# Performance work log

Measured on AMD Instinct MI355X. Metric: run time of the kernel, lower is better.

Reference implementation:

```python
import jax, jax.numpy as jnp
import numpy as np

N_NODES = 20000
N_EDGES = 320000
IN_F = 16
OUT_F = 16
EDGE_DIM = 16
EDGE_HID = 64
BN_EPS = 1e-5


def setup_inputs() -> dict:
    key = jax.random.key(0)
    ks = jax.random.split(key, 12)
    inp = {
        "h_neigh": jax.random.normal(ks[0], (N_NODES, IN_F), dtype=jnp.float32),
        "h_self": jax.random.normal(ks[1], (N_NODES, IN_F), dtype=jnp.float32),
        "edge_features": jax.random.normal(ks[2], (N_EDGES, EDGE_DIM), dtype=jnp.float32),
        "src": jax.random.randint(ks[3], (N_EDGES,), 0, N_NODES),
        "dst": jax.random.randint(ks[4], (N_EDGES,), 0, N_NODES),
        # params (xavier-ish scale)
        "W_self": jax.random.normal(ks[5], (IN_F, OUT_F), dtype=jnp.float32) * (2.0 / (IN_F + OUT_F)) ** 0.5,
        "bn_gamma": jnp.ones((OUT_F,), dtype=jnp.float32),
        "bn_beta": jnp.zeros((OUT_F,), dtype=jnp.float32),
        "We1": jax.random.normal(ks[6], (EDGE_DIM, EDGE_HID), dtype=jnp.float32) * (2.0 / (EDGE_DIM + EDGE_HID)) ** 0.5,
        "be1": jnp.zeros((EDGE_HID,), dtype=jnp.float32),
        "We2": jax.random.normal(ks[7], (EDGE_HID, IN_F * OUT_F), dtype=jnp.float32) * (2.0 / (EDGE_HID + IN_F * OUT_F)) ** 0.5,
        "be2": jnp.zeros((IN_F * OUT_F,), dtype=jnp.float32),
    }
    return inp


def reference(h_neigh, h_self, edge_features, src, dst,
              W_self, bn_gamma, bn_beta, We1, be1, We2, be2):
    n_nodes = h_self.shape[0]
    in_f, out_f = W_self.shape
    # edge MLP -> per-edge weight matrix [E, in_f, out_f]
    eh = jax.nn.relu(edge_features @ We1 + be1)
    edge_w = (eh @ We2 + be2).reshape(-1, in_f, out_f)
    # gather src features, per-edge matvec, scatter-sum to dst
    # (sum over in_f commutes with the edge sum-reduce, matching
    #  update_all(u_mul_e, sum) followed by .sum(dim=1))
    msg = jnp.einsum('ei,eio->eo', h_neigh[src], edge_w)  # [E, out_f]
    neigh = jax.ops.segment_sum(msg, dst, num_segments=n_nodes)  # [N, out_f]
    # fc_self: Linear(no bias) -> BatchNorm1d (training stats) -> tanh
    y = h_self @ W_self
    mu = y.mean(axis=0)
    var = y.var(axis=0)
    y = (y - mu) / jnp.sqrt(var + BN_EPS) * bn_gamma + bn_beta
    y = jnp.tanh(y)
    z = jax.nn.relu(y + neigh)
    z_norm = jnp.linalg.norm(z, axis=1, keepdims=True)
    z_norm = jnp.where(z_norm == 0, jnp.ones_like(z_norm), z_norm)
    return z / z_norm
```

## Files before the change

kernel.cpp:

```cpp
#include <hip/hip_runtime.h>
#include <hip/hip_bf16.h>
#include <math.h>

#define NN 20000
#define NE 320000
#define BN_EPS 1e-5f
#define CAP 48
#define CNTP 16

#define MSG_BYTES   (NE * 16 * 4)
#define ELIST_OFF   MSG_BYTES
#define ELIST_BYTES (NN * CAP * 4)
#define CNT_OFF     (ELIST_OFF + ELIST_BYTES)
#define CNT_BYTES   (NN * CNTP * 4)
#define BNACC_OFF   (CNT_OFF + CNT_BYTES)
#define Y_OFF       (BNACC_OFF + 128)
#define ZERO_OFF    CNT_OFF
#define ZERO_BYTES  (CNT_BYTES + 128)

typedef _Float16 f16x8 __attribute__((ext_vector_type(8)));
typedef float    f32x4 __attribute__((ext_vector_type(4)));

union H8 { f16x8 v; unsigned short us[8]; unsigned int ui[4]; };

__device__ __forceinline__ unsigned short f2h(float f) {
    _Float16 h = (_Float16)f;
    return __builtin_bit_cast(unsigned short, h);
}
__device__ __forceinline__ unsigned int pack2h(float a, float b) {
    return (unsigned int)f2h(a) | ((unsigned int)f2h(b) << 16);
}

__global__ __launch_bounds__(256) void bucket_kernel(
    const int* __restrict__ dst, int* __restrict__ elist, int* __restrict__ cntp)
{
    int i = (int)blockIdx.x * 256 + (int)threadIdx.x;
    if (i < NE) {
        int d0 = dst[i];
        int k0 = atomicAdd(&cntp[d0 * CNTP], 1);
        if (k0 < CAP) elist[d0 * CAP + k0] = i;
    }
}

__global__ __launch_bounds__(256, 3) void edge_kernel(
    const float* __restrict__ h_neigh, const float* __restrict__ efeat,
    const int* __restrict__ src,
    const float* __restrict__ We1, const float* __restrict__ be1,
    const float* __restrict__ We2, const float* __restrict__ be2,
    float* __restrict__ msgb,
    const float* __restrict__ h_self, const float* __restrict__ Wsf,
    float* __restrict__ y, float* __restrict__ bnacc)
{
    __shared__ __align__(16) unsigned short A3sw[16 * 2 * 64 * 8];
    __shared__ float red[4][32];

    const int t = threadIdx.x;

    {
#pragma unroll
        for (int i = 0; i < 8; i++) {
            int R = t + 256 * i;
            int co = R & 15;
            int g  = (R >> 4) & 3;
            int mbkb = R >> 6;
            int mb = mbkb >> 1, kb = mbkb & 1;
            const float* wp = We2 + (size_t)(kb * 32 + g * 8) * 256 + mb * 16 + co;
            H8 h8;
#pragma unroll
            for (int j = 0; j < 8; j++)
                h8.us[j] = f2h(wp[j * 256]);
            *(f16x8*)&A3sw[R * 8] = h8.v;
        }
    }
    __syncthreads();

    const int L = t & 63, wv = t >> 6;
    const int lo16 = L & 15, q = L >> 4;
    const int qc = q & 1;
    const bool qlow = (q < 2);
    const bool qhi1 = ((q >> 1) != 0);

    H8 w1[4];
#pragma unroll
    for (int c = 0; c < 4; c++) {
#pragma unroll
        for (int j = 0; j < 8; j++) {
            float w;
            if (q < 2)                 w = We1[(q * 8 + j) * 64 + c * 16 + lo16];
            else if (q == 2 && j == 0) w = be1[c * 16 + lo16];
            else                       w = 0.f;
            w1[c].us[j] = f2h(w);
        }
    }

    H8 be2T;
#pragma unroll
    for (int j = 0; j < 8; j++) {
        float bv = be2[(qc * 8 + j) * 16 + lo16];
        be2T.us[j] = qlow ? f2h(bv) : (unsigned short)0;
    }

    const int addrA = (((q & 1) * 2 + 0) * 16 + lo16) * 4;
    const int addrB = (((q & 1) * 2 + 1) * 16 + lo16) * 4;

    const int NT = NE / 64;
    int bt = blockIdx.x;
    {
        int e = bt * 64 + wv * 16 + lo16;
        int se = src[e];
        const float4* ep0 = (const float4*)(efeat + (size_t)e * 16 + qc * 8);
        float4 efA = ep0[0], efB = ep0[1];
        float xr[16];
        {
            const float4* xp = (const float4*)(h_neigh + (size_t)se * 16);
#pragma unroll
            for (int k4 = 0; k4 < 4; k4++) {
                float4 a = xp[k4];
                xr[k4*4+0] = a.x; xr[k4*4+1] = a.y; xr[k4*4+2] = a.z; xr[k4*4+3] = a.w;
            }
        }

        while (true) {
            int btn = bt + gridDim.x;
            bool hn = btn < NT;
            int en = 0, sen = 0;
            float4 efAn = efA, efBn = efB;
            if (hn) {
                en = btn * 64 + wv * 16 + lo16;
                sen = src[en];
                const float4* epn = (const float4*)(efeat + (size_t)en * 16 + qc * 8);
                efAn = epn[0]; efBn = epn[1];
            }

            H8 a2;
            {
                float ev[8] = {efA.x, efA.y, efA.z, efA.w, efB.x, efB.y, efB.z, efB.w};
#pragma unroll
                for (int j = 0; j < 8; j++) {
                    if (qlow) {
                        a2.us[j] = f2h(ev[j]);
                    } else {
                        a2.us[j] = (q == 2 && j == 0) ? (unsigned short)0x3C00 : (unsigned short)0;
                    }
                }
            }

            float vch[4][4];
#pragma unroll
            for (int c = 0; c < 4; c++) {
                f32x4 c2 = {0.f, 0.f, 0.f, 0.f};
                c2 = __builtin_amdgcn_mfma_f32_16x16x32_f16(w1[c].v, a2.v, c2, 0, 0, 0);
#pragma unroll
                for (int r = 0; r < 4; r++) vch[c][r] = fmaxf(c2[r], 0.f);
            }

            unsigned int dw[4][2];
#pragma unroll
            for (int c = 0; c < 4; c++) {
#pragma unroll
                for (int d = 0; d < 2; d++)
                    dw[c][d] = pack2h(vch[c][2*d], vch[c][2*d+1]);
            }

            H8 b3[2];
#pragma unroll
            for (int kb = 0; kb < 2; kb++) {
#pragma unroll
                for (int tt = 0; tt < 4; tt++) {
                    int d = tt & 1;
                    int addr = (tt >> 1) ? addrB : addrA;
                    int h0 = __builtin_amdgcn_ds_bpermute(addr, (int)dw[kb*2+0][d]);
                    int h1 = __builtin_amdgcn_ds_bpermute(addr, (int)dw[kb*2+1][d]);
                    b3[kb].ui[tt] = (unsigned int)(qhi1 ? h1 : h0);
                }
            }

            float4 nx0 = make_float4(0.f, 0.f, 0.f, 0.f), nx1 = nx0, nx2 = nx0, nx3 = nx0;
            if (hn) {
                const float4* xpn = (const float4*)(h_neigh + (size_t)sen * 16);
                nx0 = xpn[0]; nx1 = xpn[1]; nx2 = xpn[2]; nx3 = xpn[3];
            }

            H8 xT;
#pragma unroll
            for (int j = 0; j < 8; j++)
                xT.us[j] = qlow ? f2h(xr[qc * 8 + j]) : (unsigned short)0;
            f32x4 msg = {0.f, 0.f, 0.f, 0.f};
            msg = __builtin_amdgcn_mfma_f32_16x16x32_f16(be2T.v, xT.v, msg, 0, 0, 0);

#pragma unroll 4
            for (int mb = 0; mb < 16; mb++) {
                f16x8 a3a = *(const f16x8*)&A3sw[((mb * 2 + 0) * 64 + L) * 8];
                f16x8 a3b = *(const f16x8*)&A3sw[((mb * 2 + 1) * 64 + L) * 8];
                f32x4 acc = {0.f, 0.f, 0.f, 0.f};
                acc = __builtin_amdgcn_mfma_f32_16x16x32_f16(a3a, b3[0].v, acc, 0, 0, 0);
                acc = __builtin_amdgcn_mfma_f32_16x16x32_f16(a3b, b3[1].v, acc, 0, 0, 0);
                float xm = xr[mb];
                msg[0] += xm * acc[0];
                msg[1] += xm * acc[1];
                msg[2] += xm * acc[2];
                msg[3] += xm * acc[3];
            }

            *(float4*)(msgb + (size_t)e * 16 + q * 4) =
                make_float4(msg[0], msg[1], msg[2], msg[3]);

            if (!hn) break;
            bt = btn; e = en; se = sen; efA = efAn; efB = efBn;
            xr[0]  = nx0.x; xr[1]  = nx0.y; xr[2]  = nx0.z; xr[3]  = nx0.w;
            xr[4]  = nx1.x; xr[5]  = nx1.y; xr[6]  = nx1.z; xr[7]  = nx1.w;
            xr[8]  = nx2.x; xr[9]  = nx2.y; xr[10] = nx2.z; xr[11] = nx2.w;
            xr[12] = nx3.x; xr[13] = nx3.y; xr[14] = nx3.z; xr[15] = nx3.w;
        }
    }

    int sb = (int)blockIdx.x - 945;
    if (sb >= 0 && sb < 79) {
        int n = sb * 256 + t;
        bool act = (n < NN);
        float hv[16], yv[16];
        if (act) {
            const float4* h4 = (const float4*)(h_self + (size_t)n * 16);
#pragma unroll
            for (int k = 0; k < 4; k++) {
                float4 a = h4[k];
                hv[4*k+0] = a.x; hv[4*k+1] = a.y; hv[4*k+2] = a.z; hv[4*k+3] = a.w;
            }
        } else {
#pragma unroll
            for (int i = 0; i < 16; i++) hv[i] = 0.f;
        }
#pragma unroll
        for (int o = 0; o < 16; o++) {
            float a = 0.f;
#pragma unroll
            for (int i = 0; i < 16; i++) a += hv[i] * Wsf[i*16 + o];
            yv[o] = a;
        }
        if (act) {
            float4* y4 = (float4*)(y + (size_t)n * 16);
#pragma unroll
            for (int k = 0; k < 4; k++)
                y4[k] = make_float4(yv[4*k+0], yv[4*k+1], yv[4*k+2], yv[4*k+3]);
        }
        int lane = t & 63;
#pragma unroll
        for (int o = 0; o < 16; o++) {
            float a = act ? yv[o] : 0.f;
            float b = act ? yv[o]*yv[o] : 0.f;
#pragma unroll
            for (int off = 32; off > 0; off >>= 1) {
                a += __shfl_down(a, off);
                b += __shfl_down(b, off);
            }
            if (lane == 0) { red[wv][o] = a; red[wv][16 + o] = b; }
        }
        __syncthreads();
        if (t < 32) {
            float s = red[0][t] + red[1][t] + red[2][t] + red[3][t];
            atomicAdd(&bnacc[t], s);
        }
    }
}

__global__ __launch_bounds__(256) void final_kernel(
    const float* __restrict__ msgb, const int* __restrict__ elist,
    const int* __restrict__ cntp, const int* __restrict__ dst,
    const float* __restrict__ y, const float* __restrict__ bnacc,
    const float* __restrict__ gamma, const float* __restrict__ beta,
    float* __restrict__ out)
{
    int tb = blockIdx.x * 256 + threadIdx.x;
    int n = tb >> 4;
    if (n >= NN) return;
    int sub = tb & 15, s = sub >> 2, c = sub & 3;

    int deg = cntp[n * CNTP];
    const float4* m4 = (const float4*)msgb;

    float ax = 0.f, ay = 0.f, az = 0.f, aw = 0.f;
    if (deg <= CAP) {
        const int* el = elist + n * CAP;
        for (int k = s; k < deg; k += 4) {
            int e0 = el[k];
            float4 a0 = m4[(size_t)e0*4 + c];
            ax += a0.x; ay += a0.y; az += a0.z; aw += a0.w;
        }
    } else {
        for (int e0 = s; e0 < NE; e0 += 4) {
            if (dst[e0] == n) {
                float4 a0 = m4[(size_t)e0*4 + c];
                ax += a0.x; ay += a0.y; az += a0.z; aw += a0.w;
            }
        }
    }

    ax += __shfl_xor(ax, 4); ax += __shfl_xor(ax, 8);
    ay += __shfl_xor(ay, 4); ay += __shfl_xor(ay, 8);
    az += __shfl_xor(az, 4); az += __shfl_xor(az, 8);
    aw += __shfl_xor(aw, 4); aw += __shfl_xor(aw, 8);

    if (s != 0) return;

    float4 yv4 = ((const float4*)y)[(size_t)n * 4 + c];
    float yv[4] = {yv4.x, yv4.y, yv4.z, yv4.w};
    float nb[4] = {ax, ay, az, aw};

    const float inv_n = 1.f / (float)NN;
    float z[4];
    float ss = 0.f;
#pragma unroll
    for (int r = 0; r < 4; r++) {
        int o = c * 4 + r;
        float mu  = bnacc[o] * inv_n;
        float var = bnacc[16 + o] * inv_n - mu * mu;
        float inv = rsqrtf(var + BN_EPS);
        float yy  = (yv[r] - mu) * inv * gamma[o] + beta[o];
        float tt  = tanhf(yy);
        float zz  = fmaxf(tt + nb[r], 0.f);
        z[r] = zz;
        ss += zz * zz;
    }
    ss += __shfl_xor(ss, 1);
    ss += __shfl_xor(ss, 2);
    float nrm = sqrtf(ss);
    if (nrm == 0.f) nrm = 1.f;
    float rr = 1.f / nrm;
    *(float4*)(out + (size_t)n * 16 + c * 4) =
        make_float4(z[0]*rr, z[1]*rr, z[2]*rr, z[3]*rr);
}

extern "C" void kernel_launch(void* const* d_in, const int* in_sizes, int n_in,
                              void* d_out, int out_size, void* d_ws, size_t ws_size,
                              hipStream_t stream) {
    const float* h_neigh = (const float*)d_in[0];
    const float* h_self  = (const float*)d_in[1];
    const float* efeat   = (const float*)d_in[2];
    const int*   src     = (const int*)d_in[3];
    const int*   dst     = (const int*)d_in[4];
    const float* W_self  = (const float*)d_in[5];
    const float* gamma   = (const float*)d_in[6];
    const float* beta    = (const float*)d_in[7];
    const float* We1     = (const float*)d_in[8];
    const float* be1     = (const float*)d_in[9];
    const float* We2     = (const float*)d_in[10];
    const float* be2     = (const float*)d_in[11];
    float* out = (float*)d_out;

    char* ws = (char*)d_ws;
    float* msgb  = (float*)ws;
    int*   elist = (int*)(ws + ELIST_OFF);
    int*   cntp  = (int*)(ws + CNT_OFF);
    float* bnacc = (float*)(ws + BNACC_OFF);
    float* y     = (float*)(ws + Y_OFF);

    hipMemsetAsync(ws + ZERO_OFF, 0, ZERO_BYTES, stream);

    bucket_kernel<<<(NE + 255) / 256, 256, 0, stream>>>(dst, elist, cntp);
    edge_kernel<<<1024, 256, 0, stream>>>(
        h_neigh, efeat, src, We1, be1, We2, be2,
        msgb, h_self, W_self, y, bnacc);
    final_kernel<<<(NN * 16 + 255) / 256, 256, 0, stream>>>(
        msgb, elist, cntp, dst, y, bnacc, gamma, beta, out);
}
```

Baseline: 150.7 us.

## Scatter edge messages into per-destination slots instead of an edge-indexed buffer

The bucket kernel now records each edge's slot within its destination bucket, and the edge kernel writes each message directly to a per-destination contiguous region (dst*CAP + slot). The final kernel then reads messages contiguously without an edge-list indirection, and overflow edges beyond CAP are accumulated with atomics into an extra buffer instead of scanning all edges. This removes the dependent elist load and the random gather in the final reduction. In exchange the edge kernel's stores become scattered, and the workspace grows, with a sparser message buffer (NN*CAP rows) and a larger memset.

```diff
diff --git a/kernel.cpp b/kernel.cpp
--- a/kernel.cpp
+++ b/kernel.cpp
@@ -8,15 +8,17 @@
 #define CAP 48
 #define CNTP 16
 
-#define MSG_BYTES   (NE * 16 * 4)
-#define ELIST_OFF   MSG_BYTES
-#define ELIST_BYTES (NN * CAP * 4)
-#define CNT_OFF     (ELIST_OFF + ELIST_BYTES)
+#define MSG_BYTES   (NN * CAP * 16 * 4)
+#define SLOT_OFF    MSG_BYTES
+#define SLOT_BYTES  (NE * 4)
+#define CNT_OFF     (SLOT_OFF + SLOT_BYTES)
 #define CNT_BYTES   (NN * CNTP * 4)
 #define BNACC_OFF   (CNT_OFF + CNT_BYTES)
-#define Y_OFF       (BNACC_OFF + 128)
+#define EXTRA_OFF   (BNACC_OFF + 128)
+#define EXTRA_BYTES (NN * 16 * 4)
+#define Y_OFF       (EXTRA_OFF + EXTRA_BYTES)
 #define ZERO_OFF    CNT_OFF
-#define ZERO_BYTES  (CNT_BYTES + 128)
+#define ZERO_BYTES  (CNT_BYTES + 128 + EXTRA_BYTES)
 
 typedef _Float16 f16x8 __attribute__((ext_vector_type(8)));
 typedef float    f32x4 __attribute__((ext_vector_type(4)));
@@ -32,22 +34,23 @@
 }
 
 __global__ __launch_bounds__(256) void bucket_kernel(
-    const int* __restrict__ dst, int* __restrict__ elist, int* __restrict__ cntp)
+    const int* __restrict__ dst, int* __restrict__ slot, int* __restrict__ cntp)
 {
     int i = (int)blockIdx.x * 256 + (int)threadIdx.x;
     if (i < NE) {
         int d0 = dst[i];
         int k0 = atomicAdd(&cntp[d0 * CNTP], 1);
-        if (k0 < CAP) elist[d0 * CAP + k0] = i;
+        slot[i] = k0;
     }
 }
 
 __global__ __launch_bounds__(256, 3) void edge_kernel(
     const float* __restrict__ h_neigh, const float* __restrict__ efeat,
-    const int* __restrict__ src,
+    const int* __restrict__ src, const int* __restrict__ dst,
+    const int* __restrict__ slot,
     const float* __restrict__ We1, const float* __restrict__ be1,
     const float* __restrict__ We2, const float* __restrict__ be2,
-    float* __restrict__ msgb,
+    float* __restrict__ msgb, float* __restrict__ extra,
     const float* __restrict__ h_self, const float* __restrict__ Wsf,
     float* __restrict__ y, float* __restrict__ bnacc)
 {
@@ -108,6 +111,8 @@
     {
         int e = bt * 64 + wv * 16 + lo16;
         int se = src[e];
+        int de = dst[e];
+        int sl = slot[e];
         const float4* ep0 = (const float4*)(efeat + (size_t)e * 16 + qc * 8);
         float4 efA = ep0[0], efB = ep0[1];
         float xr[16];
@@ -123,11 +128,13 @@
         while (true) {
             int btn = bt + gridDim.x;
             bool hn = btn < NT;
-            int en = 0, sen = 0;
+            int en = 0, sen = 0, den = 0, sln = 0;
             float4 efAn = efA, efBn = efB;
             if (hn) {
                 en = btn * 64 + wv * 16 + lo16;
                 sen = src[en];
+                den = dst[en];
+                sln = slot[en];
                 const float4* epn = (const float4*)(efeat + (size_t)en * 16 + qc * 8);
                 efAn = epn[0]; efBn = epn[1];
             }
@@ -202,11 +209,17 @@
                 msg[3] += xm * acc[3];
             }
 
-            *(float4*)(msgb + (size_t)e * 16 + q * 4) =
-                make_float4(msg[0], msg[1], msg[2], msg[3]);
+            if (sl < CAP) {
+                *(float4*)(msgb + ((size_t)de * CAP + sl) * 16 + q * 4) =
+                    make_float4(msg[0], msg[1], msg[2], msg[3]);
+            } else {
+                float* xp2 = extra + (size_t)de * 16 + q * 4;
+#pragma unroll
+                for (int r = 0; r < 4; r++) atomicAdd(xp2 + r, msg[r]);
+            }
 
             if (!hn) break;
-            bt = btn; e = en; se = sen; efA = efAn; efB = efBn;
+            bt = btn; e = en; se = sen; de = den; sl = sln; efA = efAn; efB = efBn;
             xr[0]  = nx0.x; xr[1]  = nx0.y; xr[2]  = nx0.z; xr[3]  = nx0.w;
             xr[4]  = nx1.x; xr[5]  = nx1.y; xr[6]  = nx1.z; xr[7]  = nx1.w;
             xr[8]  = nx2.x; xr[9]  = nx2.y; xr[10] = nx2.z; xr[11] = nx2.w;
@@ -264,8 +277,8 @@
 }
 
 __global__ __launch_bounds__(256) void final_kernel(
-    const float* __restrict__ msgb, const int* __restrict__ elist,
-    const int* __restrict__ cntp, const int* __restrict__ dst,
+    const float* __restrict__ msgb, const int* __restrict__ cntp,
+    const float* __restrict__ extra,
     const float* __restrict__ y, const float* __restrict__ bnacc,
     const float* __restrict__ gamma, const float* __restrict__ beta,
     float* __restrict__ out)
@@ -276,23 +289,13 @@
     int sub = tb & 15, s = sub >> 2, c = sub & 3;
 
     int deg = cntp[n * CNTP];
-    const float4* m4 = (const float4*)msgb;
+    int m = deg < CAP ? deg : CAP;
+    const float4* base = (const float4*)(msgb + (size_t)n * CAP * 16);
 
     float ax = 0.f, ay = 0.f, az = 0.f, aw = 0.f;
-    if (deg <= CAP) {
-        const int* el = elist + n * CAP;
-        for (int k = s; k < deg; k += 4) {
-            int e0 = el[k];
-            float4 a0 = m4[(size_t)e0*4 + c];
-            ax += a0.x; ay += a0.y; az += a0.z; aw += a0.w;
-        }
-    } else {
-        for (int e0 = s; e0 < NE; e0 += 4) {
-            if (dst[e0] == n) {
-                float4 a0 = m4[(size_t)e0*4 + c];
-                ax += a0.x; ay += a0.y; az += a0.z; aw += a0.w;
-            }
-        }
+    for (int k = s; k < m; k += 4) {
+        float4 a0 = base[k * 4 + c];
+        ax += a0.x; ay += a0.y; az += a0.z; aw += a0.w;
     }
 
     ax += __shfl_xor(ax, 4); ax += __shfl_xor(ax, 8);
@@ -301,6 +304,11 @@
     aw += __shfl_xor(aw, 4); aw += __shfl_xor(aw, 8);
 
     if (s != 0) return;
+
+    if (deg > CAP) {
+        const float4 a0 = *(const float4*)(extra + (size_t)n * 16 + c * 4);
+        ax += a0.x; ay += a0.y; az += a0.z; aw += a0.w;
+    }
 
     float4 yv4 = ((const float4*)y)[(size_t)n * 4 + c];
     float yv[4] = {yv4.x, yv4.y, yv4.z, yv4.w};
@@ -349,17 +357,18 @@
 
     char* ws = (char*)d_ws;
     float* msgb  = (float*)ws;
-    int*   elist = (int*)(ws + ELIST_OFF);
+    int*   slot  = (int*)(ws + SLOT_OFF);
     int*   cntp  = (int*)(ws + CNT_OFF);
     float* bnacc = (float*)(ws + BNACC_OFF);
+    float* extra = (float*)(ws + EXTRA_OFF);
     float* y     = (float*)(ws + Y_OFF);
 
     hipMemsetAsync(ws + ZERO_OFF, 0, ZERO_BYTES, stream);
 
-    bucket_kernel<<<(NE + 255) / 256, 256, 0, stream>>>(dst, elist, cntp);
+    bucket_kernel<<<(NE + 255) / 256, 256, 0, stream>>>(dst, slot, cntp);
     edge_kernel<<<1024, 256, 0, stream>>>(
-        h_neigh, efeat, src, We1, be1, We2, be2,
-        msgb, h_self, W_self, y, bnacc);
+        h_neigh, efeat, src, dst, slot, We1, be1, We2, be2,
+        msgb, extra, h_self, W_self, y, bnacc);
     final_kernel<<<(NN * 16 + 255) / 256, 256, 0, stream>>>(
-        msgb, elist, cntp, dst, y, bnacc, gamma, beta, out);
-}
+        msgb, cntp, extra, y, bnacc, gamma, beta, out);
+}
```

Result: faster. 146.8 us (-2.5%).
